# Performance work log

Hardware: AMD Instinct MI355X
Metric: run time of the kernel (lower is better)

The kernel has to match this reference:

```python
import jax, jax.numpy as jnp
import numpy as np

EPS = 1e-06


def setup_inputs() -> dict:
    key = jax.random.key(0)
    k1, k2, k3 = jax.random.split(key, 3)
    shape = (64, 1, 480, 640)
    pred = jax.random.normal(k1, shape, dtype=jnp.float32)
    target = jax.random.normal(k2, shape, dtype=jnp.float32)
    valid_mask = jax.random.randint(k3, shape, 0, 2).astype(jnp.bool_)
    return {"pred": pred, "target": target, "valid_mask": valid_mask}


def reference(pred, target, valid_mask):
    B = pred.shape[0]
    mask = valid_mask & jnp.isfinite(pred) & jnp.isfinite(target)
    m = mask.reshape(B, -1)                      # [B, N] bool
    # Zero out invalid entries so non-finite values cannot poison reductions.
    p = jnp.where(m, pred.reshape(B, -1), 0.0)   # [B, N]
    t = jnp.where(m, target.reshape(B, -1), 0.0)  # [B, N]
    mf = m.astype(pred.dtype)

    n = mf.sum(axis=-1)                           # valid count per sample
    sum_p = p.sum(axis=-1)
    sum_t = t.sum(axis=-1)
    sum_p2 = (p * p).sum(axis=-1)
    sum_pt = (p * t).sum(axis=-1)

    det = n * sum_p2 - sum_p * sum_p
    safe = jnp.abs(det) > EPS
    det_safe = jnp.where(safe, det, 1.0)
    a = jnp.where(safe, (n * sum_pt - sum_p * sum_t) / det_safe, 1.0)
    b = jnp.where(safe, (sum_t - a * sum_p) / jnp.maximum(n, 1.0), 0.0)

    # Masked mean absolute residual per sample.
    resid = jnp.abs(a[:, None] * p + b[:, None] - t) * mf
    per_sample = resid.sum(axis=-1) / jnp.maximum(n, 1.0)

    include = (n >= 2.0).astype(pred.dtype)      # samples with < 2 valid px skipped
    cnt = include.sum()
    loss = jnp.where(cnt > 0, (per_sample * include).sum() / jnp.maximum(cnt, 1.0), 0.0)
    return loss
```

## Files before the change

### kernel.cpp

```cpp
#include <hip/hip_runtime.h>

#define B_SAMPLES 64
#define NPS       307200
#define F4PS      76800
#define BPS       30
#define F4PB      2560
#define TPB       256
#define ITERS     10
#define EPS_DET   1e-6

__device__ __forceinline__ bool finitef(float x) {
    return (__float_as_uint(x) & 0x7f800000u) != 0x7f800000u;
}

__global__ void detect_mask_layout(const uint4* __restrict__ mask,
                                   int* __restrict__ flag) {
    unsigned v = 0;
    const int base = blockIdx.x * TPB + threadIdx.x;
#pragma unroll
    for (int k = 0; k < 4; ++k) {
        uint4 m = mask[base + k * 4096];
        v |= (m.x | m.y | m.z | m.w) & 0xffffff00u;
    }
    if (v) atomicOr(flag, 1);
}

__global__ void
sums_kernel(const float* __restrict__ pred, const float* __restrict__ target,
            const void* __restrict__ mask, const int* __restrict__ flag,
            float* __restrict__ partials) {
    const int s = blockIdx.x / BPS;
    const int blk = blockIdx.x % BPS;
    const int base4 = s * F4PS + blk * F4PB + threadIdx.x;
    const bool byteLayout = (*flag != 0);

    const float4* p4 = (const float4*)pred;
    const float4* t4 = (const float4*)target;

    float n = 0.f, sp = 0.f, st = 0.f, sp2 = 0.f, spt = 0.f;

    auto accum = [&](float p, float t, bool mv) {
        bool ok = mv && finitef(p) && finitef(t);
        float pv = ok ? p : 0.f;
        float tv = ok ? t : 0.f;
        n += ok ? 1.f : 0.f;
        sp += pv;
        st += tv;
        sp2 += pv * pv;
        spt += pv * tv;
    };

    if (byteLayout) {
        const unsigned* m4 = (const unsigned*)mask;
        float4 pv[ITERS], tv[ITERS];
        unsigned mv[ITERS];
#pragma unroll
        for (int k = 0; k < ITERS; ++k) {
            const int i4 = base4 + k * TPB;
            pv[k] = p4[i4];
            tv[k] = t4[i4];
            mv[k] = m4[i4];
        }
        __builtin_amdgcn_sched_barrier(0);
#pragma unroll
        for (int k = 0; k < ITERS; ++k) {
            accum(pv[k].x, tv[k].x, (mv[k] & 0x000000ffu) != 0);
            accum(pv[k].y, tv[k].y, (mv[k] & 0x0000ff00u) != 0);
            accum(pv[k].z, tv[k].z, (mv[k] & 0x00ff0000u) != 0);
            accum(pv[k].w, tv[k].w, (mv[k] & 0xff000000u) != 0);
        }
    } else {
        const int4* m4 = (const int4*)mask;
#pragma unroll
        for (int half = 0; half < 2; ++half) {
            float4 pv[5], tv[5];
            int4 mv[5];
#pragma unroll
            for (int k = 0; k < 5; ++k) {
                const int i4 = base4 + (half * 5 + k) * TPB;
                pv[k] = p4[i4];
                tv[k] = t4[i4];
                mv[k] = m4[i4];
            }
            __builtin_amdgcn_sched_barrier(0);
#pragma unroll
            for (int k = 0; k < 5; ++k) {
                accum(pv[k].x, tv[k].x, mv[k].x != 0);
                accum(pv[k].y, tv[k].y, mv[k].y != 0);
                accum(pv[k].z, tv[k].z, mv[k].z != 0);
                accum(pv[k].w, tv[k].w, mv[k].w != 0);
            }
        }
    }

    __shared__ float red[4][5];
    const int w = threadIdx.x >> 6;
    float vals[5] = {n, sp, st, sp2, spt};
#pragma unroll
    for (int q = 0; q < 5; ++q) {
        float v = vals[q];
#pragma unroll
        for (int off = 32; off; off >>= 1) v += __shfl_xor(v, off);
        if ((threadIdx.x & 63) == 0) red[w][q] = v;
    }
    __syncthreads();
    if (threadIdx.x == 0) {
#pragma unroll
        for (int q = 0; q < 5; ++q)
            partials[(size_t)blockIdx.x * 5 + q] =
                red[0][q] + red[1][q] + red[2][q] + red[3][q];
    }
}

__global__ void
resid_kernel(const float* __restrict__ pred, const float* __restrict__ target,
             const void* __restrict__ mask, const int* __restrict__ flag,
             const float* __restrict__ partials, float* __restrict__ rpart) {
    const int s = blockIdx.x / BPS;
    const int blk = blockIdx.x % BPS;
    const int base4 = s * F4PS + blk * F4PB + threadIdx.x;
    const bool byteLayout = (*flag != 0);

    __shared__ float s_ab[2];
    if (threadIdx.x < 64) {
        const int l = threadIdx.x;
        float q0 = 0.f, q1 = 0.f, q2 = 0.f, q3 = 0.f, q4 = 0.f;
        if (l < BPS) {
            const float* q = partials + (size_t)(s * BPS + l) * 5;
            q0 = q[0]; q1 = q[1]; q2 = q[2]; q3 = q[3]; q4 = q[4];
        }
#pragma unroll
        for (int off = 32; off; off >>= 1) {
            q0 += __shfl_xor(q0, off);
            q1 += __shfl_xor(q1, off);
            q2 += __shfl_xor(q2, off);
            q3 += __shfl_xor(q3, off);
            q4 += __shfl_xor(q4, off);
        }
        if (l == 0) {
            double n = q0, sp = q1, st = q2, sp2 = q3, spt = q4;
            double det = n * sp2 - sp * sp;
            bool safe = fabs(det) > EPS_DET;
            double a = safe ? (n * spt - sp * st) / det : 1.0;
            double bb = safe ? (st - a * sp) / fmax(n, 1.0) : 0.0;
            s_ab[0] = (float)a;
            s_ab[1] = (float)bb;
        }
    }
    __syncthreads();
    const float av = s_ab[0];
    const float bv = s_ab[1];

    const float4* p4 = (const float4*)pred;
    const float4* t4 = (const float4*)target;

    float r = 0.f;
    auto accum = [&](float p, float t, bool mv) {
        bool ok = mv && finitef(p) && finitef(t);
        r += ok ? fabsf(av * p + bv - t) : 0.f;
    };

    if (byteLayout) {
        const unsigned* m4 = (const unsigned*)mask;
        float4 pv[ITERS], tv[ITERS];
        unsigned mv[ITERS];
#pragma unroll
        for (int k = 0; k < ITERS; ++k) {
            const int i4 = base4 + k * TPB;
            pv[k] = p4[i4];
            tv[k] = t4[i4];
            mv[k] = m4[i4];
        }
        __builtin_amdgcn_sched_barrier(0);
#pragma unroll
        for (int k = 0; k < ITERS; ++k) {
            accum(pv[k].x, tv[k].x, (mv[k] & 0x000000ffu) != 0);
            accum(pv[k].y, tv[k].y, (mv[k] & 0x0000ff00u) != 0);
            accum(pv[k].z, tv[k].z, (mv[k] & 0x00ff0000u) != 0);
            accum(pv[k].w, tv[k].w, (mv[k] & 0xff000000u) != 0);
        }
    } else {
        const int4* m4 = (const int4*)mask;
#pragma unroll
        for (int half = 0; half < 2; ++half) {
            float4 pv[5], tv[5];
            int4 mv[5];
#pragma unroll
            for (int k = 0; k < 5; ++k) {
                const int i4 = base4 + (half * 5 + k) * TPB;
                pv[k] = p4[i4];
                tv[k] = t4[i4];
                mv[k] = m4[i4];
            }
            __builtin_amdgcn_sched_barrier(0);
#pragma unroll
            for (int k = 0; k < 5; ++k) {
                accum(pv[k].x, tv[k].x, mv[k].x != 0);
                accum(pv[k].y, tv[k].y, mv[k].y != 0);
                accum(pv[k].z, tv[k].z, mv[k].z != 0);
                accum(pv[k].w, tv[k].w, mv[k].w != 0);
            }
        }
    }

    __shared__ float red[4];
    const int w = threadIdx.x >> 6;
    float v = r;
#pragma unroll
    for (int off = 32; off; off >>= 1) v += __shfl_xor(v, off);
    if ((threadIdx.x & 63) == 0) red[w] = v;
    __syncthreads();
    if (threadIdx.x == 0)
        rpart[blockIdx.x] = red[0] + red[1] + red[2] + red[3];
}

__global__ void final_kernel(const float* __restrict__ partials,
                             const float* __restrict__ rpart,
                             float* __restrict__ out) {
    const int s = threadIdx.x;
    double r = 0, n = 0;
    for (int b = 0; b < BPS; ++b) {
        r += (double)rpart[s * BPS + b];
        n += (double)partials[(size_t)(s * BPS + b) * 5 + 0];
    }
    double per = r / fmax(n, 1.0);
    double inc = (n >= 2.0) ? 1.0 : 0.0;
    double v = per * inc;
#pragma unroll
    for (int off = 32; off; off >>= 1) {
        v += __shfl_down(v, off);
        inc += __shfl_down(inc, off);
    }
    if (s == 0) out[0] = (float)(inc > 0.0 ? v / fmax(inc, 1.0) : 0.0);
}

extern "C" void kernel_launch(void* const* d_in, const int* in_sizes, int n_in,
                              void* d_out, int out_size, void* d_ws, size_t ws_size,
                              hipStream_t stream) {
    const float* pred = (const float*)d_in[0];
    const float* target = (const float*)d_in[1];
    const void* mask = d_in[2];
    float* out = (float*)d_out;

    int* flag = (int*)d_ws;
    float* partials = (float*)((char*)d_ws + 64);
    float* rpart = partials + (size_t)B_SAMPLES * BPS * 5;

    hipMemsetAsync(d_ws, 0, 64, stream);

    detect_mask_layout<<<16, TPB, 0, stream>>>((const uint4*)mask, flag);
    sums_kernel<<<B_SAMPLES * BPS, TPB, 0, stream>>>(pred, target, mask, flag,
                                                     partials);
    resid_kernel<<<B_SAMPLES * BPS, TPB, 0, stream>>>(pred, target, mask, flag,
                                                      partials, rpart);
    final_kernel<<<1, 64, 0, stream>>>(partials, rpart, out);
}
```

Measured before the change: 84.16 us.

## Stream inputs through LDS with double-buffered direct loads and inline layout detection

Replaces the register-batched loads with per-wave double-buffered global_load_lds staging, so the next tile's pred/target/mask fetch overlaps compute on the current tile, gated by explicit vmcnt waits. The separate layout-detect kernel and memset go away, and each block checks its own slice of the mask instead, which removes two launches. The a/b solve in resid moves from double to float precision. Risks: per-block detection could disagree across blocks on odd data, float math lowers precision of the regression solve, and each iteration now waits on in-flight loads, which limits memory-level parallelism compared with issuing all ten loads up front.

```diff
diff --git a/kernel.cpp b/kernel.cpp
--- a/kernel.cpp
+++ b/kernel.cpp
@@ -1,132 +1,162 @@
 #include <hip/hip_runtime.h>
 
 #define B_SAMPLES 64
-#define NPS       307200
 #define F4PS      76800
 #define BPS       30
 #define F4PB      2560
 #define TPB       256
 #define ITERS     10
-#define EPS_DET   1e-6
+#define WPB       4
+#define EPS_DET   1e-6f
+
+typedef __attribute__((address_space(3))) void       lds_void;
+typedef const __attribute__((address_space(1))) void gbl_void;
 
 __device__ __forceinline__ bool finitef(float x) {
     return (__float_as_uint(x) & 0x7f800000u) != 0x7f800000u;
 }
 
-__global__ void detect_mask_layout(const uint4* __restrict__ mask,
-                                   int* __restrict__ flag) {
-    unsigned v = 0;
-    const int base = blockIdx.x * TPB + threadIdx.x;
-#pragma unroll
-    for (int k = 0; k < 4; ++k) {
-        uint4 m = mask[base + k * 4096];
-        v |= (m.x | m.y | m.z | m.w) & 0xffffff00u;
-    }
-    if (v) atomicOr(flag, 1);
+__device__ __forceinline__ bool detect_byte_layout(const void* mask, int base4,
+                                                   int* sflag) {
+    const uint4* m16 =
+        (const uint4*)((const unsigned char*)mask + (size_t)base4 * 4);
+    uint4 m = m16[threadIdx.x];
+    unsigned v = (m.x | m.y | m.z | m.w) & 0xffffff00u;
+    if (threadIdx.x == 0) *sflag = 0;
+    __syncthreads();
+    if (__any(v != 0) && (threadIdx.x & 63) == 0) *sflag = 1;
+    __syncthreads();
+    return *sflag != 0;
+}
+
+__device__ __forceinline__ void stage3(const float4* gp, const float4* gt,
+                                       const unsigned* gm,
+                                       unsigned char* lbuf) {
+    __builtin_amdgcn_global_load_lds((gbl_void*)gp, (lds_void*)lbuf, 16, 0, 0);
+    __builtin_amdgcn_global_load_lds((gbl_void*)gt, (lds_void*)(lbuf + 1024),
+                                     16, 0, 0);
+    __builtin_amdgcn_global_load_lds((gbl_void*)gm, (lds_void*)(lbuf + 2048),
+                                     4, 0, 0);
 }
 
 __global__ void
 sums_kernel(const float* __restrict__ pred, const float* __restrict__ target,
-            const void* __restrict__ mask, const int* __restrict__ flag,
-            float* __restrict__ partials) {
-    const int s = blockIdx.x / BPS;
-    const int blk = blockIdx.x % BPS;
-    const int base4 = s * F4PS + blk * F4PB + threadIdx.x;
-    const bool byteLayout = (*flag != 0);
+            const void* __restrict__ mask, float* __restrict__ partials) {
+    const int s   = blockIdx.x / BPS;
+    const int sub = blockIdx.x % BPS;
+    const int base4 = s * F4PS + sub * F4PB;
+    const int tid = threadIdx.x, lane = tid & 63, w = tid >> 6;
+
+    __shared__ __align__(16) unsigned char stg[WPB][2][2304];
+    __shared__ float red[WPB][5];
+    __shared__ int sflag;
+
+    const bool byteLayout = detect_byte_layout(mask, base4, &sflag);
 
     const float4* p4 = (const float4*)pred;
     const float4* t4 = (const float4*)target;
 
     float n = 0.f, sp = 0.f, st = 0.f, sp2 = 0.f, spt = 0.f;
-
     auto accum = [&](float p, float t, bool mv) {
         bool ok = mv && finitef(p) && finitef(t);
         float pv = ok ? p : 0.f;
         float tv = ok ? t : 0.f;
-        n += ok ? 1.f : 0.f;
-        sp += pv;
-        st += tv;
+        n   += ok ? 1.f : 0.f;
+        sp  += pv;
+        st  += tv;
         sp2 += pv * pv;
         spt += pv * tv;
     };
 
     if (byteLayout) {
         const unsigned* m4 = (const unsigned*)mask;
-        float4 pv[ITERS], tv[ITERS];
-        unsigned mv[ITERS];
-#pragma unroll
-        for (int k = 0; k < ITERS; ++k) {
-            const int i4 = base4 + k * TPB;
-            pv[k] = p4[i4];
-            tv[k] = t4[i4];
-            mv[k] = m4[i4];
-        }
-        __builtin_amdgcn_sched_barrier(0);
-#pragma unroll
-        for (int k = 0; k < ITERS; ++k) {
-            accum(pv[k].x, tv[k].x, (mv[k] & 0x000000ffu) != 0);
-            accum(pv[k].y, tv[k].y, (mv[k] & 0x0000ff00u) != 0);
-            accum(pv[k].z, tv[k].z, (mv[k] & 0x00ff0000u) != 0);
-            accum(pv[k].w, tv[k].w, (mv[k] & 0xff000000u) != 0);
+        unsigned char* buf0 = &stg[w][0][0];
+        unsigned char* buf1 = &stg[w][1][0];
+        const int i0 = base4 + w * 64 + lane;
+        stage3(p4 + i0, t4 + i0, m4 + i0, buf0);
+#pragma unroll
+        for (int t = 0; t < ITERS; ++t) {
+            unsigned char* cur = (t & 1) ? buf1 : buf0;
+            unsigned char* nxt = (t & 1) ? buf0 : buf1;
+            if (t < ITERS - 1) {
+                const int i4 = i0 + (t + 1) * TPB;
+                stage3(p4 + i4, t4 + i4, m4 + i4, nxt);
+                __builtin_amdgcn_sched_barrier(0);
+                asm volatile("s_waitcnt vmcnt(3)" ::: "memory");
+            } else {
+                __builtin_amdgcn_sched_barrier(0);
+                asm volatile("s_waitcnt vmcnt(0)" ::: "memory");
+            }
+            __builtin_amdgcn_sched_barrier(0);
+            const float4  pv = *(const float4*)(cur + (size_t)lane * 16);
+            const float4  tv = *(const float4*)(cur + 1024 + (size_t)lane * 16);
+            const unsigned mm = *(const unsigned*)(cur + 2048 + (size_t)lane * 4);
+            accum(pv.x, tv.x, (mm & 0x000000ffu) != 0);
+            accum(pv.y, tv.y, (mm & 0x0000ff00u) != 0);
+            accum(pv.z, tv.z, (mm & 0x00ff0000u) != 0);
+            accum(pv.w, tv.w, (mm & 0xff000000u) != 0);
         }
     } else {
         const int4* m4 = (const int4*)mask;
-#pragma unroll
-        for (int half = 0; half < 2; ++half) {
-            float4 pv[5], tv[5];
-            int4 mv[5];
-#pragma unroll
-            for (int k = 0; k < 5; ++k) {
-                const int i4 = base4 + (half * 5 + k) * TPB;
-                pv[k] = p4[i4];
-                tv[k] = t4[i4];
-                mv[k] = m4[i4];
-            }
-            __builtin_amdgcn_sched_barrier(0);
-#pragma unroll
-            for (int k = 0; k < 5; ++k) {
-                accum(pv[k].x, tv[k].x, mv[k].x != 0);
-                accum(pv[k].y, tv[k].y, mv[k].y != 0);
-                accum(pv[k].z, tv[k].z, mv[k].z != 0);
-                accum(pv[k].w, tv[k].w, mv[k].w != 0);
-            }
-        }
-    }
-
-    __shared__ float red[4][5];
-    const int w = threadIdx.x >> 6;
-    float vals[5] = {n, sp, st, sp2, spt};
-#pragma unroll
-    for (int q = 0; q < 5; ++q) {
-        float v = vals[q];
-#pragma unroll
-        for (int off = 32; off; off >>= 1) v += __shfl_xor(v, off);
-        if ((threadIdx.x & 63) == 0) red[w][q] = v;
-    }
-    __syncthreads();
-    if (threadIdx.x == 0) {
-#pragma unroll
-        for (int q = 0; q < 5; ++q)
-            partials[(size_t)blockIdx.x * 5 + q] =
-                red[0][q] + red[1][q] + red[2][q] + red[3][q];
+        for (int t = 0; t < ITERS; ++t) {
+            const int i4 = base4 + t * TPB + tid;
+            float4 p = p4[i4]; float4 tt = t4[i4]; int4 mm = m4[i4];
+            accum(p.x, tt.x, mm.x != 0);
+            accum(p.y, tt.y, mm.y != 0);
+            accum(p.z, tt.z, mm.z != 0);
+            accum(p.w, tt.w, mm.w != 0);
+        }
+    }
+
+    {
+        float vals[5] = {n, sp, st, sp2, spt};
+#pragma unroll
+        for (int q = 0; q < 5; ++q) {
+            float v = vals[q];
+#pragma unroll
+            for (int off = 32; off; off >>= 1) v += __shfl_xor(v, off);
+            if (lane == 0) red[w][q] = v;
+        }
+        __syncthreads();
+        if (tid == 0) {
+#pragma unroll
+            for (int q = 0; q < 5; ++q)
+                partials[(size_t)blockIdx.x * 5 + q] =
+                    red[0][q] + red[1][q] + red[2][q] + red[3][q];
+        }
     }
 }
 
 __global__ void
 resid_kernel(const float* __restrict__ pred, const float* __restrict__ target,
-             const void* __restrict__ mask, const int* __restrict__ flag,
-             const float* __restrict__ partials, float* __restrict__ rpart) {
-    const int s = blockIdx.x / BPS;
-    const int blk = blockIdx.x % BPS;
-    const int base4 = s * F4PS + blk * F4PB + threadIdx.x;
-    const bool byteLayout = (*flag != 0);
-
+             const void* __restrict__ mask, const float* __restrict__ partials,
+             float* __restrict__ rpart) {
+    const int s   = blockIdx.x / BPS;
+    const int sub = blockIdx.x % BPS;
+    const int base4 = s * F4PS + sub * F4PB;
+    const int tid = threadIdx.x, lane = tid & 63, w = tid >> 6;
+
+    __shared__ __align__(16) unsigned char stg[WPB][2][2304];
+    __shared__ float red[WPB];
     __shared__ float s_ab[2];
-    if (threadIdx.x < 64) {
-        const int l = threadIdx.x;
+    __shared__ int sflag;
+
+    const bool byteLayout = detect_byte_layout(mask, base4, &sflag);
+
+    const float4* p4 = (const float4*)pred;
+    const float4* t4 = (const float4*)target;
+    const unsigned* m4b = (const unsigned*)mask;
+
+    unsigned char* buf0 = &stg[w][0][0];
+    unsigned char* buf1 = &stg[w][1][0];
+    const int i0 = base4 + w * 64 + lane;
+    if (byteLayout)
+        stage3(p4 + i0, t4 + i0, m4b + i0, buf0);
+
+    if (tid < 64) {
         float q0 = 0.f, q1 = 0.f, q2 = 0.f, q3 = 0.f, q4 = 0.f;
-        if (l < BPS) {
-            const float* q = partials + (size_t)(s * BPS + l) * 5;
+        if (tid < BPS) {
+            const float* q = partials + (size_t)(s * BPS + tid) * 5;
             q0 = q[0]; q1 = q[1]; q2 = q[2]; q3 = q[3]; q4 = q[4];
         }
 #pragma unroll
@@ -137,81 +167,69 @@
             q3 += __shfl_xor(q3, off);
             q4 += __shfl_xor(q4, off);
         }
-        if (l == 0) {
-            double n = q0, sp = q1, st = q2, sp2 = q3, spt = q4;
-            double det = n * sp2 - sp * sp;
-            bool safe = fabs(det) > EPS_DET;
-            double a = safe ? (n * spt - sp * st) / det : 1.0;
-            double bb = safe ? (st - a * sp) / fmax(n, 1.0) : 0.0;
-            s_ab[0] = (float)a;
-            s_ab[1] = (float)bb;
+        if (tid == 0) {
+            float det = q0 * q3 - q1 * q1;
+            bool safe = fabsf(det) > EPS_DET;
+            float a  = safe ? (q0 * q4 - q1 * q2) / det : 1.f;
+            float bb = safe ? (q2 - a * q1) / fmaxf(q0, 1.f) : 0.f;
+            s_ab[0] = a;
+            s_ab[1] = bb;
         }
     }
     __syncthreads();
     const float av = s_ab[0];
     const float bv = s_ab[1];
 
-    const float4* p4 = (const float4*)pred;
-    const float4* t4 = (const float4*)target;
-
     float r = 0.f;
-    auto accum = [&](float p, float t, bool mv) {
+    auto raccum = [&](float p, float t, bool mv) {
         bool ok = mv && finitef(p) && finitef(t);
         r += ok ? fabsf(av * p + bv - t) : 0.f;
     };
 
     if (byteLayout) {
-        const unsigned* m4 = (const unsigned*)mask;
-        float4 pv[ITERS], tv[ITERS];
-        unsigned mv[ITERS];
-#pragma unroll
-        for (int k = 0; k < ITERS; ++k) {
-            const int i4 = base4 + k * TPB;
-            pv[k] = p4[i4];
-            tv[k] = t4[i4];
-            mv[k] = m4[i4];
-        }
-        __builtin_amdgcn_sched_barrier(0);
-#pragma unroll
-        for (int k = 0; k < ITERS; ++k) {
-            accum(pv[k].x, tv[k].x, (mv[k] & 0x000000ffu) != 0);
-            accum(pv[k].y, tv[k].y, (mv[k] & 0x0000ff00u) != 0);
-            accum(pv[k].z, tv[k].z, (mv[k] & 0x00ff0000u) != 0);
-            accum(pv[k].w, tv[k].w, (mv[k] & 0xff000000u) != 0);
+#pragma unroll
+        for (int t = 0; t < ITERS; ++t) {
+            unsigned char* cur = (t & 1) ? buf1 : buf0;
+            unsigned char* nxt = (t & 1) ? buf0 : buf1;
+            if (t < ITERS - 1) {
+                const int i4 = i0 + (t + 1) * TPB;
+                stage3(p4 + i4, t4 + i4, m4b + i4, nxt);
+                __builtin_amdgcn_sched_barrier(0);
+                asm volatile("s_waitcnt vmcnt(3)" ::: "memory");
+            } else {
+                __builtin_amdgcn_sched_barrier(0);
+                asm volatile("s_waitcnt vmcnt(0)" ::: "memory");
+            }
+            __builtin_amdgcn_sched_barrier(0);
+            const float4  pv = *(const float4*)(cur + (size_t)lane * 16);
+            const float4  tv = *(const float4*)(cur + 1024 + (size_t)lane * 16);
+            const unsigned mm = *(const unsigned*)(cur + 2048 + (size_t)lane * 4);
+            raccum(pv.x, tv.x, (mm & 0x000000ffu) != 0);
+            raccum(pv.y, tv.y, (mm & 0x0000ff00u) != 0);
+            raccum(pv.z, tv.z, (mm & 0x00ff0000u) != 0);
+            raccum(pv.w, tv.w, (mm & 0xff000000u) != 0);
         }
     } else {
         const int4* m4 = (const int4*)mask;
-#pragma unroll
-        for (int half = 0; half < 2; ++half) {
-            float4 pv[5], tv[5];
-            int4 mv[5];
-#pragma unroll
-            for (int k = 0; k < 5; ++k) {
-                const int i4 = base4 + (half * 5 + k) * TPB;
-                pv[k] = p4[i4];
-                tv[k] = t4[i4];
-                mv[k] = m4[i4];
-            }
-            __builtin_amdgcn_sched_barrier(0);
-#pragma unroll
-            for (int k = 0; k < 5; ++k) {
-                accum(pv[k].x, tv[k].x, mv[k].x != 0);
-                accum(pv[k].y, tv[k].y, mv[k].y != 0);
-                accum(pv[k].z, tv[k].z, mv[k].z != 0);
-                accum(pv[k].w, tv[k].w, mv[k].w != 0);
-            }
-        }
-    }
-
-    __shared__ float red[4];
-    const int w = threadIdx.x >> 6;
-    float v = r;
-#pragma unroll
-    for (int off = 32; off; off >>= 1) v += __shfl_xor(v, off);
-    if ((threadIdx.x & 63) == 0) red[w] = v;
-    __syncthreads();
-    if (threadIdx.x == 0)
-        rpart[blockIdx.x] = red[0] + red[1] + red[2] + red[3];
+        for (int t = 0; t < ITERS; ++t) {
+            const int i4 = base4 + t * TPB + tid;
+            float4 p = p4[i4]; float4 tt = t4[i4]; int4 mm = m4[i4];
+            raccum(p.x, tt.x, mm.x != 0);
+            raccum(p.y, tt.y, mm.y != 0);
+            raccum(p.z, tt.z, mm.z != 0);
+            raccum(p.w, tt.w, mm.w != 0);
+        }
+    }
+
+    {
+        float v = r;
+#pragma unroll
+        for (int off = 32; off; off >>= 1) v += __shfl_xor(v, off);
+        if (lane == 0) red[w] = v;
+        __syncthreads();
+        if (tid == 0)
+            rpart[blockIdx.x] = red[0] + red[1] + red[2] + red[3];
+    }
 }
 
 __global__ void final_kernel(const float* __restrict__ partials,
@@ -242,16 +260,12 @@
     const void* mask = d_in[2];
     float* out = (float*)d_out;
 
-    int* flag = (int*)d_ws;
-    float* partials = (float*)((char*)d_ws + 64);
+    float* partials = (float*)d_ws;
     float* rpart = partials + (size_t)B_SAMPLES * BPS * 5;
 
-    hipMemsetAsync(d_ws, 0, 64, stream);
-
-    detect_mask_layout<<<16, TPB, 0, stream>>>((const uint4*)mask, flag);
-    sums_kernel<<<B_SAMPLES * BPS, TPB, 0, stream>>>(pred, target, mask, flag,
+    sums_kernel<<<B_SAMPLES * BPS, TPB, 0, stream>>>(pred, target, mask,
                                                      partials);
-    resid_kernel<<<B_SAMPLES * BPS, TPB, 0, stream>>>(pred, target, mask, flag,
+    resid_kernel<<<B_SAMPLES * BPS, TPB, 0, stream>>>(pred, target, mask,
                                                       partials, rpart);
     final_kernel<<<1, 64, 0, stream>>>(partials, rpart, out);
 }
```

Result: faster. 79.94 us (-5.0%).
